# Performance work log

Hardware: AMD Instinct MI355X
Metric: run time of the kernel (lower is better)

Reference implementation:

```python
import jax, jax.numpy as jnp
import numpy as np

N, E, D_IN, H, C, E_DIM, FF = 50000, 800000, 128, 8, 16, 16, 512
HC = H * C
LAMBDA_INIT = 0.8
NEG = 0.2
EPS = 1e-5


def setup_inputs() -> dict:
    key = jax.random.key(0)
    ks = jax.random.split(key, 24)
    n = lambda k, s, sc=1.0: jax.random.normal(k, s, dtype=jnp.float32) * sc
    return {
        "x": n(ks[0], (N, D_IN)),
        "edge_attr": n(ks[1], (E, E_DIM)),
        "W_l1": n(ks[2], (D_IN, HC), 0.05),
        "W_l2": n(ks[3], (D_IN, HC), 0.05),
        "att_l1": n(ks[4], (1, H, C), 0.1),
        "att_r1": n(ks[5], (1, H, C), 0.1),
        "att_l2": n(ks[6], (1, H, C), 0.1),
        "att_r2": n(ks[7], (1, H, C), 0.1),
        "W_e1": n(ks[8], (E_DIM, HC), 0.1),
        "att_e1": n(ks[9], (1, H, C), 0.1),
        "W_e2": n(ks[10], (E_DIM, HC), 0.1),
        "att_e2": n(ks[11], (1, H, C), 0.1),
        "lq1": n(ks[12], (H, C), 0.1),
        "lk1": n(ks[13], (H, C), 0.1),
        "lq2": n(ks[14], (H, C), 0.1),
        "lk2": n(ks[15], (H, C), 0.1),
        "rms_attn": jnp.ones((HC,), jnp.float32),
        "W_out": n(ks[16], (HC, HC), 0.05),
        "b_out": jnp.zeros((HC,), jnp.float32),
        "bias_extra": jnp.zeros((HC,), jnp.float32),
        "rms_layer": jnp.ones((HC,), jnp.float32),
        "W_ff1": n(ks[17], (HC, FF), 0.05),
        "b_ff1": jnp.zeros((FF,), jnp.float32),
        "W_ff2": n(ks[18], (FF, HC), 0.05),
        "b_ff2": jnp.zeros((HC,), jnp.float32),
        "edge_index": jax.random.randint(ks[19], (2, E), 0, N, dtype=jnp.int32),
    }


def _rmsnorm(x, scale):
    norm = jnp.sqrt(jnp.mean(x * x, axis=-1, keepdims=True) + EPS)
    return x / norm * scale


def _forward(x, edge_attr, W_l1, W_l2, att_l1, att_r1, att_l2, att_r2,
             W_e1, att_e1, W_e2, att_e2, lq1, lk1, lq2, lk2,
             rms_attn, W_out, b_out, bias_extra, rms_layer,
             W_ff1, b_ff1, W_ff2, b_ff2, edge_index):
    src0, dst0 = edge_index[0], edge_index[1]
    # add_self_loops(fill_value='mean'): self-loop edge_attr = mean of incoming edge attrs
    deg = jax.ops.segment_sum(jnp.ones((E,), x.dtype), dst0, num_segments=N)
    loop_attr = jax.ops.segment_sum(edge_attr, dst0, num_segments=N) / jnp.maximum(deg, 1.0)[:, None]
    ar = jnp.arange(N, dtype=src0.dtype)
    src = jnp.concatenate([src0, ar])
    dst = jnp.concatenate([dst0, ar])
    ea = jnp.concatenate([edge_attr, loop_attr], axis=0)  # [E+N, edge_dim]

    def attn_pass(xh, att_l, att_r, W_e, att_e):
        e = (ea @ W_e).reshape(-1, H, C)          # [E2, H, C]
        xi = xh[dst]                               # target features [E2,H,C]
        xj = xh[src]                               # source features [E2,H,C]
        alpha = (xi * att_l).sum(-1) + (xj * att_r).sum(-1) + (e * att_e).sum(-1)  # [E2,H]
        alpha = jnp.where(alpha >= 0, alpha, NEG * alpha)  # leaky_relu
        amax = jax.ops.segment_max(alpha, dst, num_segments=N)
        alpha = jnp.exp(alpha - amax[dst])
        denom = jax.ops.segment_sum(alpha, dst, num_segments=N)
        alpha = alpha / denom[dst]
        return jax.ops.segment_sum((xj + e) * alpha[..., None], dst, num_segments=N)  # [N,H,C]

    x1 = (x @ W_l1).reshape(N, H, C)
    x2 = (x @ W_l2).reshape(N, H, C)
    out1 = attn_pass(x1, att_l1, att_r1, W_e1, att_e1)
    out2 = attn_pass(x2, att_l2, att_r2, W_e2, att_e2)

    lam = jnp.exp((lq1 * lk1).sum(-1)) - jnp.exp((lq2 * lk2).sum(-1)) + LAMBDA_INIT  # [H]
    out = (out1 - lam[None, :, None] * out2).reshape(N, HC)
    out = _rmsnorm(out, rms_attn) * (1.0 - LAMBDA_INIT)
    out = out @ W_out + b_out + bias_extra

    # transformer layer: residual + pre-norm FFN
    h = x + out
    hn = _rmsnorm(h, rms_layer)
    ff = jax.nn.gelu(hn @ W_ff1 + b_ff1, approximate=False) @ W_ff2 + b_ff2
    return h + ff


def reference(x, edge_attr, W_l1, W_l2, att_l1, att_r1, att_l2, att_r2,
              W_e1, att_e1, W_e2, att_e2, lq1, lk1, lq2, lk2,
              rms_attn, W_out, b_out, bias_extra, rms_layer,
              W_ff1, b_ff1, W_ff2, b_ff2, edge_index):
    return _forward(x, edge_attr, W_l1, W_l2, att_l1, att_r1, att_l2, att_r2,
                    W_e1, att_e1, W_e2, att_e2, lq1, lk1, lq2, lk2,
                    rms_attn, W_out, b_out, bias_extra, rms_layer,
                    W_ff1, b_ff1, W_ff2, b_ff2, edge_index)
```

## Files before the change

### kernel.cpp

```cpp
#include <hip/hip_runtime.h>
#include <math.h>

constexpr int N_  = 50000;
constexpr int E_  = 800000;
constexpr int H_  = 8;
constexpr int C_  = 16;
constexpr int HC_ = 128;
constexpr int ED_ = 16;
constexpr int FF_ = 512;
constexpr int NT_ = 3125;
constexpr float NEG_ = 0.2f;
constexpr float EPS_ = 1e-5f;
constexpr float LAMBDA_INIT_ = 0.8f;
constexpr float LOG2E_ = 1.4426950408889634f;

typedef __attribute__((ext_vector_type(8))) short bf16x8;
typedef __attribute__((ext_vector_type(4))) float f32x4;
typedef __fp16 half2v __attribute__((ext_vector_type(2)));

__device__ __forceinline__ float gelu_exact(float v) {
    return 0.5f * v * (1.0f + erff(v * 0.70710678118654752440f));
}
__device__ __forceinline__ ushort f2bf(float f) {
    uint u = __float_as_uint(f);
    return (ushort)((u + 0x7FFFu + ((u >> 16) & 1u)) >> 16);
}
__device__ __forceinline__ ushort f2h(float f) {
    __fp16 h = (__fp16)f;
    return *(ushort*)&h;
}
__device__ __forceinline__ uint pkh2(float a, float b) {
    half2v h = __builtin_amdgcn_cvt_pkrtz(a, b);
    return *(uint*)&h;
}
__device__ __forceinline__ void uph2(uint u, float& a, float& b) {
    half2v h = *(half2v*)&u;
    a = (float)h.x; b = (float)h.y;
}

constexpr int XC_   = N_ * HC_ / 4;
constexpr int WL12_ = 288 * 128;
constexpr int WO_   = 128 * 128;
constexpr int WF1_  = 512 * 128;
constexpr int WF2_  = 128 * 512;
constexpr int CVT_TOTAL_ = XC_ + WL12_ + WO_ + WF1_ + WF2_ + 128 + 8 + E_;

__device__ void wconv(const float* __restrict__ W, ushort* __restrict__ Wt, int t, int K, int N) {
    int col = t / K, k = t - col * K;
    Wt[t] = f2bf(W[(size_t)k * N + col]);
}
__device__ void wconv_h(const float* __restrict__ W, ushort* __restrict__ Wt, int t, int K, int N) {
    int col = t / K, k = t - col * K;
    Wt[t] = f2h(W[(size_t)k * N + col]);
}

__global__ __launch_bounds__(256) void k_cvt(const float* __restrict__ x,
        const float* __restrict__ Wl1, const float* __restrict__ al1w, const float* __restrict__ ar1w,
        const float* __restrict__ Wl2, const float* __restrict__ al2w, const float* __restrict__ ar2w,
        const float* __restrict__ Wout, const float* __restrict__ Wff1, const float* __restrict__ Wff2,
        const float* __restrict__ We1, const float* __restrict__ ae1,
        const float* __restrict__ We2, const float* __restrict__ ae2,
        const float* __restrict__ lq1, const float* __restrict__ lk1,
        const float* __restrict__ lq2, const float* __restrict__ lk2,
        const int* __restrict__ dst0,
        ushort* __restrict__ xb, ushort* __restrict__ wl12t,
        ushort* __restrict__ woutt, ushort* __restrict__ wff1t, ushort* __restrict__ wff2t,
        float2* __restrict__ wc, float* __restrict__ lam,
        int* __restrict__ deg, int* __restrict__ rank) {
    int g = blockIdx.x * blockDim.x + threadIdx.x;
    if (g < XC_) {
        float4 v = ((const float4*)x)[g];
        ushort4 o;
        o.x = f2bf(v.x); o.y = f2bf(v.y); o.z = f2bf(v.z); o.w = f2bf(v.w);
        ((ushort4*)xb)[g] = o;
        return;
    }
    g -= XC_;
    if (g < WL12_) {
        int col = g >> 7, k = g & 127;
        const float* W = (col < 144) ? Wl1 : Wl2;
        const float* alw = (col < 144) ? al1w : al2w;
        const float* arw = (col < 144) ? ar1w : ar2w;
        int c = (col < 144) ? col : col - 144;
        float v;
        if (c < 128) {
            v = W[(size_t)k * HC_ + c];
        } else if (c < 136) {
            int h = c - 128; v = 0.f;
#pragma unroll
            for (int cc = 0; cc < 16; ++cc) v = fmaf(W[(size_t)k * HC_ + h * 16 + cc], alw[h * 16 + cc], v);
        } else {
            int h = c - 136; v = 0.f;
#pragma unroll
            for (int cc = 0; cc < 16; ++cc) v = fmaf(W[(size_t)k * HC_ + h * 16 + cc], arw[h * 16 + cc], v);
        }
        wl12t[g] = f2bf(v);
        return;
    }
    g -= WL12_;
    if (g < WO_) { wconv(Wout, woutt, g, 128, 128); return; }
    g -= WO_;
    if (g < WF1_) { wconv(Wff1, wff1t, g, 128, 512); return; }
    g -= WF1_;
    if (g < WF2_) { wconv_h(Wff2, wff2t, g, 512, 128); return; }
    g -= WF2_;
    if (g < 128) {
        int k = g >> 3, h = g & 7;
        float s1 = 0.f, s2 = 0.f;
#pragma unroll
        for (int c = 0; c < 16; ++c) {
            s1 = fmaf(We1[k * HC_ + h * 16 + c], ae1[h * 16 + c], s1);
            s2 = fmaf(We2[k * HC_ + h * 16 + c], ae2[h * 16 + c], s2);
        }
        wc[g] = make_float2(s1, s2);
        return;
    }
    g -= 128;
    if (g < 8) {
        float d1 = 0.f, d2 = 0.f;
#pragma unroll
        for (int k = 0; k < 16; ++k) {
            d1 = fmaf(lq1[g * 16 + k], lk1[g * 16 + k], d1);
            d2 = fmaf(lq2[g * 16 + k], lk2[g * 16 + k], d2);
        }
        lam[g] = __expf(d1) - __expf(d2) + LAMBDA_INIT_;
        return;
    }
    g -= 8;
    if (g < E_) {
        rank[g] = atomicAdd(&deg[dst0[g]], 1);
    }
}

__global__ __launch_bounds__(1024) void k_scan(const int* __restrict__ deg,
                                               int* __restrict__ offs) {
    __shared__ int part[1024];
    int t = threadIdx.x;
    const int CH = (N_ + 1023) / 1024;
    int b = t * CH;
    int e = min(N_, b + CH);
    int sum = 0;
    for (int i = b; i < e; ++i) sum += deg[i];
    part[t] = sum;
    __syncthreads();
    for (int off = 1; off < 1024; off <<= 1) {
        int v = (t >= off) ? part[t - off] : 0;
        __syncthreads();
        part[t] += v;
        __syncthreads();
    }
    int run = (t == 0) ? 0 : part[t - 1];
    for (int i = b; i < e; ++i) {
        offs[i] = run;
        run += deg[i];
    }
    if (t == 1023) offs[N_] = run;
}

__global__ __launch_bounds__(256) void k_et(const float* __restrict__ eattr,
                                            const float2* __restrict__ all_,
                                            const float2* __restrict__ arr_,
                                            const float2* __restrict__ wc,
                                            const int* __restrict__ offs,
                                            const int* __restrict__ rank,
                                            const int* __restrict__ src0,
                                            const int* __restrict__ dst0,
                                            uint* __restrict__ rec,
                                            int* __restrict__ csr_src) {
    __shared__ float2 wcs[128];
    int t = threadIdx.x;
    if (t < 128) wcs[t] = wc[t];
    __syncthreads();
    int e = blockIdx.x * blockDim.x + t;
    if (e >= E_) return;
    const float* ea = eattr + (size_t)e * ED_;
    float eav[16];
    {
        float4 q0 = *(const float4*)(ea + 0);
        float4 q1 = *(const float4*)(ea + 4);
        float4 q2 = *(const float4*)(ea + 8);
        float4 q3 = *(const float4*)(ea + 12);
        eav[0] = q0.x; eav[1] = q0.y; eav[2] = q0.z; eav[3] = q0.w;
        eav[4] = q1.x; eav[5] = q1.y; eav[6] = q1.z; eav[7] = q1.w;
        eav[8] = q2.x; eav[9] = q2.y; eav[10] = q2.z; eav[11] = q2.w;
        eav[12] = q3.x; eav[13] = q3.y; eav[14] = q3.z; eav[15] = q3.w;
    }
    int src = src0[e], dst = dst0[e];
    const float2* alp = all_ + (size_t)dst * 8;
    const float2* arp = arr_ + (size_t)src * 8;
    uint ra[8], re[8];
#pragma unroll
    for (int h = 0; h < 8; ++h) {
        float t1 = 0.f, t2 = 0.f;
#pragma unroll
        for (int k = 0; k < 16; ++k) {
            float2 w = wcs[k * 8 + h];
            t1 = fmaf(eav[k], w.x, t1);
            t2 = fmaf(eav[k], w.y, t2);
        }
        float2 al = alp[h], ar = arp[h];
        float a1 = al.x + ar.x + t1;
        a1 = ((a1 >= 0.f) ? a1 : NEG_ * a1) * LOG2E_;
        float a2 = al.y + ar.y + t2;
        a2 = ((a2 >= 0.f) ? a2 : NEG_ * a2) * LOG2E_;
        ra[h] = pkh2(a1, a2);
    }
#pragma unroll
    for (int i = 0; i < 8; ++i) re[i] = pkh2(eav[2 * i], eav[2 * i + 1]);
    int p = offs[dst] + rank[e];
    csr_src[p] = src;
    uint4* rp = (uint4*)(rec + (size_t)p * 16);
    rp[0] = make_uint4(ra[0], ra[1], ra[2], ra[3]);
    rp[1] = make_uint4(ra[4], ra[5], ra[6], ra[7]);
    rp[2] = make_uint4(re[0], re[1], re[2], re[3]);
    rp[3] = make_uint4(re[4], re[5], re[6], re[7]);
}

__global__ __launch_bounds__(256) void k_agg(const ushort* __restrict__ x12,
                                             const float2* __restrict__ all_,
                                             const float2* __restrict__ arr_,
                                             const uint* __restrict__ rec,
                                             const float2* __restrict__ wcg,
                                             const float* __restrict__ We1, const float* __restrict__ We2,
                                             const float* __restrict__ lam, const float* __restrict__ rms_attn,
                                             const int* __restrict__ offs, const int* __restrict__ csr_src,
                                             ushort* __restrict__ attn_out) {
    int wid = (int)((blockIdx.x * blockDim.x + threadIdx.x) >> 6);
    if (wid >= N_) return;
    int lane = threadIdx.x & 63;
    int h = lane >> 3;
    int cp = lane & 7;
    int e0 = h * C_ + cp * 2;
    int hbase = lane & 56;

    int s = offs[wid], eend = offs[wid + 1];
    int deg = eend - s;

    float s1 = 0.f, s2 = 0.f;
    float ax1x = 0.f, ax1y = 0.f, ax2x = 0.f, ax2y = 0.f;
    float ws1x = 0.f, ws1y = 0.f, ws2x = 0.f, ws2y = 0.f;
    float esx = 0.f, esy = 0.f;

    auto edge_step = [&](int j) {
        int src = csr_src[j];
        const uint* r = rec + (size_t)j * 16;
        uint ua = r[h];
        uint ue = r[8 + cp];
        uint2 ux = *(const uint2*)(x12 + (size_t)src * 256 + e0 * 2);
        float a1, a2, eax, eay, x1a, x2a, x1b, x2b;
        uph2(ua, a1, a2);
        uph2(ue, eax, eay);
        uph2(ux.x, x1a, x2a);
        uph2(ux.y, x1b, x2b);
        float p1 = exp2f(a1), p2 = exp2f(a2);
        s1 += p1; s2 += p2;
        ax1x = fmaf(p1, x1a, ax1x); ax1y = fmaf(p1, x1b, ax1y);
        ax2x = fmaf(p2, x2a, ax2x); ax2y = fmaf(p2, x2b, ax2y);
        ws1x = fmaf(p1, eax, ws1x); ws1y = fmaf(p1, eay, ws1y);
        ws2x = fmaf(p2, eax, ws2x); ws2y = fmaf(p2, eay, ws2y);
        esx += eax; esy += eay;
    };

    int j = s;
    for (; j + 1 < eend; j += 2) {
        edge_step(j);
        edge_step(j + 1);
    }
    if (j < eend) edge_step(j);

    float invdeg = 1.0f / (float)max(deg, 1);
    float esmx = esx * invdeg, esmy = esy * invdeg;

    float2 w0 = wcg[(2 * cp) * 8 + h];
    float2 w1 = wcg[(2 * cp + 1) * 8 + h];
    float tp1 = esmx * w0.x + esmy * w1.x;
    float tp2 = esmx * w0.y + esmy * w1.y;
    tp1 += __shfl_xor(tp1, 1); tp1 += __shfl_xor(tp1, 2); tp1 += __shfl_xor(tp1, 4);
    tp2 += __shfl_xor(tp2, 1); tp2 += __shfl_xor(tp2, 2); tp2 += __shfl_xor(tp2, 4);

    float2 alv = all_[(size_t)wid * 8 + h];
    float2 arv = arr_[(size_t)wid * 8 + h];
    float aS1 = alv.x + arv.x + tp1;
    aS1 = ((aS1 >= 0.f) ? aS1 : NEG_ * aS1) * LOG2E_;
    float aS2 = alv.y + arv.y + tp2;
    aS2 = ((aS2 >= 0.f) ? aS2 : NEG_ * aS2) * LOG2E_;
    float pS1 = exp2f(aS1), pS2 = exp2f(aS2);
    {
        uint2 ux = *(const uint2*)(x12 + (size_t)wid * 256 + e0 * 2);
        float x1a, x2a, x1b, x2b;
        uph2(ux.x, x1a, x2a);
        uph2(ux.y, x1b, x2b);
        s1 += pS1; s2 += pS2;
        ax1x = fmaf(pS1, x1a, ax1x); ax1y = fmaf(pS1, x1b, ax1y);
        ax2x = fmaf(pS2, x2a, ax2x); ax2y = fmaf(pS2, x2b, ax2y);
        ws1x = fmaf(pS1, esmx, ws1x); ws1y = fmaf(pS1, esmy, ws1y);
        ws2x = fmaf(pS2, esmx, ws2x); ws2y = fmaf(pS2, esmy, ws2y);
    }

    float o1x = ax1x, o1y = ax1y, o2x = ax2x, o2y = ax2y;
#pragma unroll
    for (int kp = 0; kp < 8; ++kp) {
        float wa1 = __shfl(ws1x, hbase + kp), wb1 = __shfl(ws1y, hbase + kp);
        float wa2 = __shfl(ws2x, hbase + kp), wb2 = __shfl(ws2y, hbase + kp);
        float2 a0 = *(const float2*)(We1 + (2 * kp) * HC_ + e0);
        float2 a1 = *(const float2*)(We1 + (2 * kp + 1) * HC_ + e0);
        float2 b0 = *(const float2*)(We2 + (2 * kp) * HC_ + e0);
        float2 b1 = *(const float2*)(We2 + (2 * kp + 1) * HC_ + e0);
        o1x = fmaf(wa1, a0.x, o1x); o1x = fmaf(wb1, a1.x, o1x);
        o1y = fmaf(wa1, a0.y, o1y); o1y = fmaf(wb1, a1.y, o1y);
        o2x = fmaf(wa2, b0.x, o2x); o2x = fmaf(wb2, b1.x, o2x);
        o2y = fmaf(wa2, b0.y, o2y); o2y = fmaf(wb2, b1.y, o2y);
    }
    float inv1 = 1.0f / s1, inv2 = 1.0f / s2;
    o1x *= inv1; o1y *= inv1; o2x *= inv2; o2y *= inv2;

    float lamh = lam[h];
    float v0 = o1x - lamh * o2x;
    float v1 = o1y - lamh * o2y;

    float ss = v0 * v0 + v1 * v1;
#pragma unroll
    for (int mk = 1; mk < 64; mk <<= 1) ss += __shfl_xor(ss, mk);
    float rn = rsqrtf(ss * (1.0f / 128.0f) + EPS_);
    float g0 = rms_attn[e0] * (1.0f - LAMBDA_INIT_);
    float g1 = rms_attn[e0 + 1] * (1.0f - LAMBDA_INIT_);
    ushort2 o;
    o.x = f2bf(v0 * rn * g0);
    o.y = f2bf(v1 * rn * g1);
    *(ushort2*)(attn_out + (size_t)wid * HC_ + e0) = o;
}

__global__ __launch_bounds__(256) void k_g0(const ushort* __restrict__ xb,
                                            const ushort* __restrict__ wl12t,
                                            ushort* __restrict__ x12,
                                            float* __restrict__ alr,
                                            float* __restrict__ arr) {
    int tid = threadIdx.x;
    int w = tid >> 6, lane = tid & 63;
    int lrow = lane & 15, kg = lane >> 4;
    int cg = w & 1, rh = w >> 1;

    bf16x8 B[9][4];
#pragma unroll
    for (int c = 0; c < 9; ++c) {
        int ct = cg * 9 + c;
#pragma unroll
        for (int ks = 0; ks < 4; ++ks)
            B[c][ks] = *(const bf16x8*)(wl12t + (size_t)(ct * 16 + lrow) * 128 + ks * 32 + kg * 8);
    }

    for (int tile = blockIdx.x * 2 + rh; tile < NT_; tile += gridDim.x * 2) {
        int r0 = tile * 16;
        const ushort* Ap = xb + (size_t)(r0 + lrow) * 128 + kg * 8;
        bf16x8 af[4];
#pragma unroll
        for (int ks = 0; ks < 4; ++ks) af[ks] = *(const bf16x8*)(Ap + ks * 32);
        f32x4 acc[9];
#pragma unroll
        for (int c = 0; c < 9; ++c) acc[c] = (f32x4){0.f, 0.f, 0.f, 0.f};
#pragma unroll
        for (int ks = 0; ks < 4; ++ks)
#pragma unroll
            for (int c = 0; c < 9; ++c)
                acc[c] = __builtin_amdgcn_mfma_f32_16x16x32_bf16(af[ks], B[c][ks], acc[c], 0, 0, 0);

#pragma unroll
        for (int c = 0; c < 8; ++c) {
            int col = c * 16 + lrow;
#pragma unroll
            for (int jj = 0; jj < 4; ++jj) {
                int r = r0 + kg * 4 + jj;
                x12[(size_t)r * 256 + col * 2 + cg] = f2h(acc[c][jj]);
            }
        }
#pragma unroll
        for (int jj = 0; jj < 4; ++jj) {
            int r = r0 + kg * 4 + jj;
            float v = acc[8][jj];
            if (lrow < 8) alr[((size_t)r * 8 + lrow) * 2 + cg] = v;
            else          arr[((size_t)r * 8 + (lrow - 8)) * 2 + cg] = v;
        }
    }
}

__global__ __launch_bounds__(256) void k_g1(const ushort* __restrict__ attn,
                                            const ushort* __restrict__ woutt,
                                            const float* __restrict__ b1,
                                            const float* __restrict__ b2,
                                            const float* __restrict__ res,
                                            const float* __restrict__ scale,
                                            float* __restrict__ hbuf,
                                            ushort* __restrict__ hn) {
    int tid = threadIdx.x;
    int w = tid >> 6, lane = tid & 63;
    int lrow = lane & 15, kg = lane >> 4;

    bf16x8 B[8][4];
#pragma unroll
    for (int c = 0; c < 8; ++c)
#pragma unroll
        for (int ks = 0; ks < 4; ++ks)
            B[c][ks] = *(const bf16x8*)(woutt + (size_t)(c * 16 + lrow) * 128 + ks * 32 + kg * 8);

    for (int tile = blockIdx.x * 4 + w; tile < NT_; tile += gridDim.x * 4) {
        int r0 = tile * 16;
        const ushort* Ap = attn + (size_t)(r0 + lrow) * 128 + kg * 8;
        bf16x8 af[4];
#pragma unroll
        for (int ks = 0; ks < 4; ++ks) af[ks] = *(const bf16x8*)(Ap + ks * 32);
        f32x4 acc[8];
#pragma unroll
        for (int c = 0; c < 8; ++c) acc[c] = (f32x4){0.f, 0.f, 0.f, 0.f};
#pragma unroll
        for (int ks = 0; ks < 4; ++ks)
#pragma unroll
            for (int c = 0; c < 8; ++c)
                acc[c] = __builtin_amdgcn_mfma_f32_16x16x32_bf16(af[ks], B[c][ks], acc[c], 0, 0, 0);

        float ssj[4] = {0.f, 0.f, 0.f, 0.f};
#pragma unroll
        for (int c = 0; c < 8; ++c) {
            int col = c * 16 + lrow;
            float bv = b1[col] + b2[col];
#pragma unroll
            for (int jj = 0; jj < 4; ++jj) {
                int r = r0 + kg * 4 + jj;
                float v = acc[c][jj] + bv + res[(size_t)r * HC_ + col];
                acc[c][jj] = v;
                ssj[jj] += v * v;
            }
        }
        float rn[4];
#pragma unroll
        for (int jj = 0; jj < 4; ++jj) {
            float ss = ssj[jj];
            ss += __shfl_xor(ss, 1); ss += __shfl_xor(ss, 2);
            ss += __shfl_xor(ss, 4); ss += __shfl_xor(ss, 8);
            rn[jj] = rsqrtf(ss * (1.0f / 128.0f) + EPS_);
        }
#pragma unroll
        for (int c = 0; c < 8; ++c) {
            int col = c * 16 + lrow;
            float sc = scale[col];
#pragma unroll
            for (int jj = 0; jj < 4; ++jj) {
                int r = r0 + kg * 4 + jj;
                float v = acc[c][jj];
                hbuf[(size_t)r * HC_ + col] = v;
                hn[(size_t)r * HC_ + col] = f2bf(v * rn[jj] * sc);
            }
        }
    }
}

__global__ __launch_bounds__(256) void k_ff1(const ushort* __restrict__ hn,
                                             const ushort* __restrict__ wff1t,
                                             const float* __restrict__ bff1,
                                             ushort* __restrict__ g) {
    int tid = threadIdx.x;
    int w = tid >> 6, lane = tid & 63;
    int lrow = lane & 15, kg = lane >> 4;

    bf16x8 B[8][4];
#pragma unroll
    for (int c = 0; c < 8; ++c)
#pragma unroll
        for (int ks = 0; ks < 4; ++ks)
            B[c][ks] = *(const bf16x8*)(wff1t + (size_t)(w * 128 + c * 16 + lrow) * 128 + ks * 32 + kg * 8);

    for (int tile = blockIdx.x; tile < NT_; tile += gridDim.x) {
        int r0 = tile * 16;
        const ushort* Ap = hn + (size_t)(r0 + lrow) * 128 + kg * 8;
        bf16x8 af[4];
#pragma unroll
        for (int ks = 0; ks < 4; ++ks) af[ks] = *(const bf16x8*)(Ap + ks * 32);
        f32x4 acc[8];
#pragma unroll
        for (int c = 0; c < 8; ++c) acc[c] = (f32x4){0.f, 0.f, 0.f, 0.f};
#pragma unroll
        for (int ks = 0; ks < 4; ++ks)
#pragma unroll
            for (int c = 0; c < 8; ++c)
                acc[c] = __builtin_amdgcn_mfma_f32_16x16x32_bf16(af[ks], B[c][ks], acc[c], 0, 0, 0);

#pragma unroll
        for (int c = 0; c < 8; ++c) {
            int col = w * 128 + c * 16 + lrow;
            float bv = bff1[col];
#pragma unroll
            for (int jj = 0; jj < 4; ++jj) {
                float v = gelu_exact(acc[c][jj] + bv);
                float other = __shfl_xor(v, 1);
                if (!(lrow & 1)) {
                    int r = r0 + kg * 4 + jj;
                    ((uint*)g)[(size_t)r * 256 + (col >> 1)] = pkh2(v, other);
                }
            }
        }
    }
}

__global__ __launch_bounds__(256) void k_ff2(const ushort* __restrict__ g,
                                             const ushort* __restrict__ wff2t,
                                             const float* __restrict__ bff2,
                                             const float* __restrict__ hres,
                                             float* __restrict__ out) {
    int tid = threadIdx.x;
    int w = tid >> 6, lane = tid & 63;
    int lrow = lane & 15, kg = lane >> 4;

    bf16x8 B[2][16];
#pragma unroll
    for (int c = 0; c < 2; ++c)
#pragma unroll
        for (int ks = 0; ks < 16; ++ks)
            B[c][ks] = *(const bf16x8*)(wff2t + (size_t)((2 * w + c) * 16 + lrow) * 512 + ks * 32 + kg * 8);

    for (int tile = blockIdx.x; tile < NT_; tile += gridDim.x) {
        int r0 = tile * 16;
        const ushort* Ap = g + (size_t)(r0 + lrow) * 512 + kg * 8;
        f32x4 acc[2];
        acc[0] = (f32x4){0.f, 0.f, 0.f, 0.f};
        acc[1] = (f32x4){0.f, 0.f, 0.f, 0.f};
#pragma unroll
        for (int ks = 0; ks < 16; ++ks) {
            bf16x8 af = *(const bf16x8*)(Ap + ks * 32);
            acc[0] = __builtin_amdgcn_mfma_f32_16x16x32_f16(af, B[0][ks], acc[0], 0, 0, 0);
            acc[1] = __builtin_amdgcn_mfma_f32_16x16x32_f16(af, B[1][ks], acc[1], 0, 0, 0);
        }
#pragma unroll
        for (int c = 0; c < 2; ++c) {
            int col = (2 * w + c) * 16 + lrow;
            float bv = bff2[col];
#pragma unroll
            for (int jj = 0; jj < 4; ++jj) {
                int r = r0 + kg * 4 + jj;
                out[(size_t)r * HC_ + col] = acc[c][jj] + bv + hres[(size_t)r * HC_ + col];
            }
        }
    }
}

extern "C" void kernel_launch(void* const* d_in, const int* in_sizes, int n_in,
                              void* d_out, int out_size, void* d_ws, size_t ws_size,
                              hipStream_t stream) {
    const float* x        = (const float*)d_in[0];
    const float* eattr    = (const float*)d_in[1];
    const float* W_l1     = (const float*)d_in[2];
    const float* W_l2     = (const float*)d_in[3];
    const float* att_l1   = (const float*)d_in[4];
    const float* att_r1   = (const float*)d_in[5];
    const float* att_l2   = (const float*)d_in[6];
    const float* att_r2   = (const float*)d_in[7];
    const float* W_e1     = (const float*)d_in[8];
    const float* att_e1   = (const float*)d_in[9];
    const float* W_e2     = (const float*)d_in[10];
    const float* att_e2   = (const float*)d_in[11];
    const float* lq1      = (const float*)d_in[12];
    const float* lk1      = (const float*)d_in[13];
    const float* lq2      = (const float*)d_in[14];
    const float* lk2      = (const float*)d_in[15];
    const float* rms_attn = (const float*)d_in[16];
    const float* W_out    = (const float*)d_in[17];
    const float* b_out    = (const float*)d_in[18];
    const float* bias_x   = (const float*)d_in[19];
    const float* rms_layer= (const float*)d_in[20];
    const float* W_ff1    = (const float*)d_in[21];
    const float* b_ff1    = (const float*)d_in[22];
    const float* W_ff2    = (const float*)d_in[23];
    const float* b_ff2    = (const float*)d_in[24];
    const int*   eidx     = (const int*)d_in[25];
    const int* src0 = eidx;
    const int* dst0 = eidx + E_;
    float* out = (float*)d_out;

    char* base = (char*)d_ws;
    size_t off = 0;
    auto alloc = [&](size_t bytes) -> char* {
        off = (off + 255) & ~(size_t)255;
        char* p = base + off;
        off += bytes;
        return p;
    };
    const size_t NF = (size_t)N_ * HC_;
    float*  f_h    = (float*)alloc(NF * 4);
    ushort* f_hnat = (ushort*)alloc(NF * 2);
    ushort* f_x12  = (ushort*)alloc(NF * 2 * 2);
    char*   f_rg   = alloc((size_t)E_ * 64);
    uint*   f_rec  = (uint*)f_rg;
    ushort* f_g    = (ushort*)f_rg;
    ushort* f_xb   = (ushort*)alloc(NF * 2);
    ushort* w_l12t = (ushort*)alloc((size_t)288 * 128 * 2);
    ushort* w_outt = (ushort*)alloc((size_t)HC_ * HC_ * 2);
    ushort* w_ff1t = (ushort*)alloc((size_t)HC_ * FF_ * 2);
    ushort* w_ff2t = (ushort*)alloc((size_t)FF_ * HC_ * 2);
    float2* f_all  = (float2*)alloc((size_t)N_ * H_ * 8);
    float2* f_arr  = (float2*)alloc((size_t)N_ * H_ * 8);
    float2* f_wc   = (float2*)alloc(128 * 8);
    float*  f_lam  = (float*)alloc(256);
    int*  i_deg  = (int*)alloc((size_t)N_ * 4);
    int*  i_offs = (int*)alloc((size_t)(N_ + 1) * 4);
    int*  i_rank = (int*)alloc((size_t)E_ * 4);
    int*  i_csr  = (int*)alloc((size_t)E_ * 4);
    (void)ws_size;

    hipMemsetAsync(i_deg, 0, (size_t)N_ * 4, stream);

    k_cvt<<<dim3((CVT_TOTAL_ + 255) / 256), dim3(256), 0, stream>>>(
        x, W_l1, att_l1, att_r1, W_l2, att_l2, att_r2, W_out, W_ff1, W_ff2,
        W_e1, att_e1, W_e2, att_e2, lq1, lk1, lq2, lk2, dst0,
        f_xb, w_l12t, w_outt, w_ff1t, w_ff2t, f_wc, f_lam, i_deg, i_rank);

    k_scan<<<dim3(1), dim3(1024), 0, stream>>>(i_deg, i_offs);

    k_g0<<<dim3(512), dim3(256), 0, stream>>>(f_xb, w_l12t, f_x12,
                                              (float*)f_all, (float*)f_arr);

    k_et<<<dim3(E_ / 256), dim3(256), 0, stream>>>(eattr, f_all, f_arr, f_wc,
                                                   i_offs, i_rank, src0, dst0,
                                                   f_rec, i_csr);

    k_agg<<<dim3((N_ + 3) / 4), dim3(256), 0, stream>>>(
        f_x12, f_all, f_arr, f_rec, f_wc,
        W_e1, W_e2, f_lam, rms_attn, i_offs, i_csr, f_hnat);

    k_g1<<<dim3(256), dim3(256), 0, stream>>>(f_hnat, w_outt, b_out, bias_x, x,
                                              rms_layer, f_h, f_hnat);

    k_ff1<<<dim3(512), dim3(256), 0, stream>>>(f_hnat, w_ff1t, b_ff1, f_g);
    k_ff2<<<dim3(1024), dim3(256), 0, stream>>>(f_g, w_ff2t, b_ff2, f_h, out);
}
```

Baseline: 444.2 us.

## Fuse x bf16 conversion into GEMM load and reorder edge pass to CSR order

Removes the separate bf16 copy of x by converting fp32 rows inside the first GEMM's operand load, avoiding a full intermediate write and read. Adds a fill kernel that builds CSR-ordered (dst, edge id, src) arrays so the edge-transform kernel writes its records contiguously instead of scattering them. In exchange, edge attributes are gathered randomly and an extra kernel launch and pass over the edge arrays are added.

```diff
diff --git a/kernel.cpp b/kernel.cpp
--- a/kernel.cpp
+++ b/kernel.cpp
@@ -38,12 +38,11 @@
     a = (float)h.x; b = (float)h.y;
 }
 
-constexpr int XC_   = N_ * HC_ / 4;
 constexpr int WL12_ = 288 * 128;
 constexpr int WO_   = 128 * 128;
 constexpr int WF1_  = 512 * 128;
 constexpr int WF2_  = 128 * 512;
-constexpr int CVT_TOTAL_ = XC_ + WL12_ + WO_ + WF1_ + WF2_ + 128 + 8 + E_;
+constexpr int CVT_TOTAL_ = WL12_ + WO_ + WF1_ + WF2_ + 128 + 8 + E_;
 
 __device__ void wconv(const float* __restrict__ W, ushort* __restrict__ Wt, int t, int K, int N) {
     int col = t / K, k = t - col * K;
@@ -54,7 +53,7 @@
     Wt[t] = f2h(W[(size_t)k * N + col]);
 }
 
-__global__ __launch_bounds__(256) void k_cvt(const float* __restrict__ x,
+__global__ __launch_bounds__(256) void k_cvt(
         const float* __restrict__ Wl1, const float* __restrict__ al1w, const float* __restrict__ ar1w,
         const float* __restrict__ Wl2, const float* __restrict__ al2w, const float* __restrict__ ar2w,
         const float* __restrict__ Wout, const float* __restrict__ Wff1, const float* __restrict__ Wff2,
@@ -63,19 +62,11 @@
         const float* __restrict__ lq1, const float* __restrict__ lk1,
         const float* __restrict__ lq2, const float* __restrict__ lk2,
         const int* __restrict__ dst0,
-        ushort* __restrict__ xb, ushort* __restrict__ wl12t,
+        ushort* __restrict__ wl12t,
         ushort* __restrict__ woutt, ushort* __restrict__ wff1t, ushort* __restrict__ wff2t,
         float2* __restrict__ wc, float* __restrict__ lam,
         int* __restrict__ deg, int* __restrict__ rank) {
     int g = blockIdx.x * blockDim.x + threadIdx.x;
-    if (g < XC_) {
-        float4 v = ((const float4*)x)[g];
-        ushort4 o;
-        o.x = f2bf(v.x); o.y = f2bf(v.y); o.z = f2bf(v.z); o.w = f2bf(v.w);
-        ((ushort4*)xb)[g] = o;
-        return;
-    }
-    g -= XC_;
     if (g < WL12_) {
         int col = g >> 7, k = g & 127;
         const float* W = (col < 144) ? Wl1 : Wl2;
@@ -157,23 +148,37 @@
     if (t == 1023) offs[N_] = run;
 }
 
+__global__ __launch_bounds__(256) void k_fill(const int* __restrict__ src0,
+                                              const int* __restrict__ dst0,
+                                              const int* __restrict__ offs,
+                                              const int* __restrict__ rank,
+                                              int* __restrict__ csr_src,
+                                              int2* __restrict__ csr_de) {
+    int e = blockIdx.x * blockDim.x + threadIdx.x;
+    if (e >= E_) return;
+    int d = dst0[e];
+    int p = offs[d] + rank[e];
+    csr_src[p] = src0[e];
+    csr_de[p] = make_int2(d, e);
+}
+
 __global__ __launch_bounds__(256) void k_et(const float* __restrict__ eattr,
                                             const float2* __restrict__ all_,
                                             const float2* __restrict__ arr_,
                                             const float2* __restrict__ wc,
-                                            const int* __restrict__ offs,
-                                            const int* __restrict__ rank,
-                                            const int* __restrict__ src0,
-                                            const int* __restrict__ dst0,
-                                            uint* __restrict__ rec,
-                                            int* __restrict__ csr_src) {
+                                            const int* __restrict__ csr_src,
+                                            const int2* __restrict__ csr_de,
+                                            uint* __restrict__ rec) {
     __shared__ float2 wcs[128];
     int t = threadIdx.x;
     if (t < 128) wcs[t] = wc[t];
     __syncthreads();
-    int e = blockIdx.x * blockDim.x + t;
-    if (e >= E_) return;
-    const float* ea = eattr + (size_t)e * ED_;
+    int p = blockIdx.x * blockDim.x + t;
+    if (p >= E_) return;
+    int2 de = csr_de[p];
+    int dst = de.x, eid = de.y;
+    int src = csr_src[p];
+    const float* ea = eattr + (size_t)eid * ED_;
     float eav[16];
     {
         float4 q0 = *(const float4*)(ea + 0);
@@ -185,7 +190,6 @@
         eav[8] = q2.x; eav[9] = q2.y; eav[10] = q2.z; eav[11] = q2.w;
         eav[12] = q3.x; eav[13] = q3.y; eav[14] = q3.z; eav[15] = q3.w;
     }
-    int src = src0[e], dst = dst0[e];
     const float2* alp = all_ + (size_t)dst * 8;
     const float2* arp = arr_ + (size_t)src * 8;
     uint ra[8], re[8];
@@ -207,8 +211,6 @@
     }
 #pragma unroll
     for (int i = 0; i < 8; ++i) re[i] = pkh2(eav[2 * i], eav[2 * i + 1]);
-    int p = offs[dst] + rank[e];
-    csr_src[p] = src;
     uint4* rp = (uint4*)(rec + (size_t)p * 16);
     rp[0] = make_uint4(ra[0], ra[1], ra[2], ra[3]);
     rp[1] = make_uint4(ra[4], ra[5], ra[6], ra[7]);
@@ -330,7 +332,7 @@
     *(ushort2*)(attn_out + (size_t)wid * HC_ + e0) = o;
 }
 
-__global__ __launch_bounds__(256) void k_g0(const ushort* __restrict__ xb,
+__global__ __launch_bounds__(256) void k_g0(const float* __restrict__ x,
                                             const ushort* __restrict__ wl12t,
                                             ushort* __restrict__ x12,
                                             float* __restrict__ alr,
@@ -351,10 +353,19 @@
 
     for (int tile = blockIdx.x * 2 + rh; tile < NT_; tile += gridDim.x * 2) {
         int r0 = tile * 16;
-        const ushort* Ap = xb + (size_t)(r0 + lrow) * 128 + kg * 8;
+        const float* Ap = x + (size_t)(r0 + lrow) * 128 + kg * 8;
         bf16x8 af[4];
 #pragma unroll
-        for (int ks = 0; ks < 4; ++ks) af[ks] = *(const bf16x8*)(Ap + ks * 32);
+        for (int ks = 0; ks < 4; ++ks) {
+            float4 qa = *(const float4*)(Ap + ks * 32);
+            float4 qb = *(const float4*)(Ap + ks * 32 + 4);
+            bf16x8 t;
+            t[0] = (short)f2bf(qa.x); t[1] = (short)f2bf(qa.y);
+            t[2] = (short)f2bf(qa.z); t[3] = (short)f2bf(qa.w);
+            t[4] = (short)f2bf(qb.x); t[5] = (short)f2bf(qb.y);
+            t[6] = (short)f2bf(qb.z); t[7] = (short)f2bf(qb.w);
+            af[ks] = t;
+        }
         f32x4 acc[9];
 #pragma unroll
         for (int c = 0; c < 9; ++c) acc[c] = (f32x4){0.f, 0.f, 0.f, 0.f};
@@ -589,7 +600,6 @@
     char*   f_rg   = alloc((size_t)E_ * 64);
     uint*   f_rec  = (uint*)f_rg;
     ushort* f_g    = (ushort*)f_rg;
-    ushort* f_xb   = (ushort*)alloc(NF * 2);
     ushort* w_l12t = (ushort*)alloc((size_t)288 * 128 * 2);
     ushort* w_outt = (ushort*)alloc((size_t)HC_ * HC_ * 2);
     ushort* w_ff1t = (ushort*)alloc((size_t)HC_ * FF_ * 2);
@@ -602,23 +612,25 @@
     int*  i_offs = (int*)alloc((size_t)(N_ + 1) * 4);
     int*  i_rank = (int*)alloc((size_t)E_ * 4);
     int*  i_csr  = (int*)alloc((size_t)E_ * 4);
+    int2* i_de   = (int2*)alloc((size_t)E_ * 8);
     (void)ws_size;
 
     hipMemsetAsync(i_deg, 0, (size_t)N_ * 4, stream);
 
     k_cvt<<<dim3((CVT_TOTAL_ + 255) / 256), dim3(256), 0, stream>>>(
-        x, W_l1, att_l1, att_r1, W_l2, att_l2, att_r2, W_out, W_ff1, W_ff2,
+        W_l1, att_l1, att_r1, W_l2, att_l2, att_r2, W_out, W_ff1, W_ff2,
         W_e1, att_e1, W_e2, att_e2, lq1, lk1, lq2, lk2, dst0,
-        f_xb, w_l12t, w_outt, w_ff1t, w_ff2t, f_wc, f_lam, i_deg, i_rank);
+        w_l12t, w_outt, w_ff1t, w_ff2t, f_wc, f_lam, i_deg, i_rank);
 
     k_scan<<<dim3(1), dim3(1024), 0, stream>>>(i_deg, i_offs);
-
-    k_g0<<<dim3(512), dim3(256), 0, stream>>>(f_xb, w_l12t, f_x12,
+    k_fill<<<dim3((E_ + 255) / 256), dim3(256), 0, stream>>>(src0, dst0, i_offs, i_rank,
+                                                             i_csr, i_de);
+
+    k_g0<<<dim3(512), dim3(256), 0, stream>>>(x, w_l12t, f_x12,
                                               (float*)f_all, (float*)f_arr);
 
     k_et<<<dim3(E_ / 256), dim3(256), 0, stream>>>(eattr, f_all, f_arr, f_wc,
-                                                   i_offs, i_rank, src0, dst0,
-                                                   f_rec, i_csr);
+                                                   i_csr, i_de, f_rec);
 
     k_agg<<<dim3((N_ + 3) / 4), dim3(256), 0, stream>>>(
         f_x12, f_all, f_arr, f_rec, f_wc,
```

After: 448.9 us. Within noise of the previous version (+1.1%).
